# Performance work log

Measured on AMD Instinct MI355X. Metric: run time of the kernel, lower is better.

## Reference

```python
import jax, jax.numpy as jnp
import numpy as np

N = 32768      # total nodes
B = 64         # graphs
NPG = 512      # nodes per graph
E = 524288     # edges (avg degree 16)
H = 4          # heads
Fh = 64        # per-head dim
C = H * Fh     # 256
FIN = 128
RATIO = 0.5


def gat(x, src, dst, W, a_src, a_dst, bias, n_nodes):
    # PyG GATConv: linear -> add self-loops -> edge softmax over dst -> scatter-add
    h = (x @ W).reshape(n_nodes, H, Fh)
    loop = jnp.arange(n_nodes)
    s = jnp.concatenate([src, loop])
    d = jnp.concatenate([dst, loop])
    es = jnp.sum(h * a_src, axis=-1)  # [N,H]
    ed = jnp.sum(h * a_dst, axis=-1)  # [N,H]
    e = jax.nn.leaky_relu(es[s] + ed[d], 0.2)  # [E+N,H]
    m = jax.ops.segment_max(e, d, num_segments=n_nodes)
    ex = jnp.exp(e - m[d])
    den = jax.ops.segment_sum(ex, d, num_segments=n_nodes)
    alpha = ex / (den[d] + 1e-16)  # [E+N,H]
    out = jax.ops.segment_sum(alpha[:, :, None] * h[s], d, num_segments=n_nodes)
    return out.reshape(n_nodes, C) + bias


def pool(x, sw, sb, tw, tb, n_graphs, n_per):
    # equal-size graphs -> per-graph top-k as a batched top_k
    k = max(1, int(n_per * RATIO))
    scores = jax.nn.sigmoid(x @ sw + sb)[:, 0].reshape(n_graphs, n_per)
    _, idx = jax.lax.top_k(scores, k)  # [B,k]
    xb = x.reshape(n_graphs, n_per, x.shape[-1])
    sel = jnp.take_along_axis(xb, idx[:, :, None], axis=1)
    sel = sel.reshape(n_graphs * k, x.shape[-1])
    return sel @ tw + tb, k


def setup_inputs() -> dict:
    key = jax.random.key(0)
    ks = jax.random.split(key, 24)
    x = jax.random.normal(ks[0], (N, FIN), dtype=jnp.float32)
    # within-graph random edges
    gbase = jnp.repeat(jnp.arange(B, dtype=jnp.int32) * NPG, E // B)
    src = gbase + jax.random.randint(ks[1], (E,), 0, NPG)
    dst = gbase + jax.random.randint(ks[2], (E,), 0, NPG)
    edge_index = jnp.stack([src, dst]).astype(jnp.int32)
    batch = jnp.repeat(jnp.arange(B, dtype=jnp.int32), NPG)
    def lin(k, fi, fo):
        return jax.random.normal(k, (fi, fo), dtype=jnp.float32) / np.sqrt(fi)
    inp = dict(x=x, edge_index=edge_index, batch=batch)
    inp["W1"] = lin(ks[3], FIN, C)
    inp["a_src1"] = jax.random.normal(ks[4], (H, Fh), jnp.float32) / np.sqrt(Fh)
    inp["a_dst1"] = jax.random.normal(ks[5], (H, Fh), jnp.float32) / np.sqrt(Fh)
    inp["b1"] = jnp.zeros((C,), jnp.float32)
    inp["W2"] = lin(ks[6], C, C)
    inp["a_src2"] = jax.random.normal(ks[7], (H, Fh), jnp.float32) / np.sqrt(Fh)
    inp["a_dst2"] = jax.random.normal(ks[8], (H, Fh), jnp.float32) / np.sqrt(Fh)
    inp["b2"] = jnp.zeros((C,), jnp.float32)
    inp["p1_sw"] = lin(ks[9], C, 1)
    inp["p1_sb"] = jnp.zeros((1,), jnp.float32)
    inp["p1_tw"] = lin(ks[10], C, C)
    inp["p1_tb"] = jnp.zeros((C,), jnp.float32)
    inp["p2_sw"] = lin(ks[11], C, 1)
    inp["p2_sb"] = jnp.zeros((1,), jnp.float32)
    inp["p2_tw"] = lin(ks[12], C, C)
    inp["p2_tb"] = jnp.zeros((C,), jnp.float32)
    inp["c1w"] = lin(ks[13], C, 64)
    inp["c1b"] = jnp.zeros((64,), jnp.float32)
    inp["c2w"] = lin(ks[14], 64, 2)
    inp["c2b"] = jnp.zeros((2,), jnp.float32)
    return inp


def reference(x, edge_index, batch, W1, a_src1, a_dst1, b1, W2, a_src2, a_dst2, b2,
              p1_sw, p1_sb, p1_tw, p1_tb, p2_sw, p2_sb, p2_tw, p2_tb,
              c1w, c1b, c2w, c2b):
    src, dst = edge_index[0], edge_index[1]
    h = jax.nn.elu(gat(x, src, dst, W1, a_src1, a_dst1, b1, N))
    h = jax.nn.elu(gat(h, src, dst, W2, a_src2, a_dst2, b2, N))
    # pool1 then pool2 (edge_index after pooling is never consumed by the output path)
    h, k1 = pool(h, p1_sw, p1_sb, p1_tw, p1_tb, B, NPG)
    h, k2 = pool(h, p2_sw, p2_sb, p2_tw, p2_tb, B, k1)
    g = h.reshape(B, k2, C).mean(axis=1)  # global mean pool per graph
    g = jax.nn.relu(g @ c1w + c1b)
    g = g @ c2w + c2b
    return jax.nn.log_softmax(g, axis=1)
```

## Files before the change

### kernel.cpp

```cpp
#include <hip/hip_runtime.h>
#include <hip/hip_bf16.h>
#include <hip/hip_fp16.h>
#include <math.h>

constexpr int NN  = 32768;
constexpr int BG  = 64;
constexpr int NPG = 512;
constexpr int EG  = 524288;
constexpr int EPG = EG / BG;
constexpr int HH  = 4;
constexpr int FH  = 64;
constexpr int CC  = 256;
constexpr int FIN = 128;
constexpr int KP1 = 256;
constexpr int KP2 = 128;
constexpr int NS  = 4;

typedef __attribute__((ext_vector_type(8))) short short8;
typedef __attribute__((ext_vector_type(4))) float f32x4;
typedef __attribute__((ext_vector_type(2))) float f32x2v;

__device__ inline float leaky02(float v) { return v > 0.0f ? v : 0.2f * v; }

__device__ inline unsigned short f2bf(float v) {
    __hip_bfloat16 h = __float2bfloat16(v);
    return *(unsigned short*)&h;
}
__device__ inline float bf2f(unsigned short u) {
    __hip_bfloat16 h;
    *(unsigned short*)&h = u;
    return __bfloat162float(h);
}
__device__ inline void split2(float v, unsigned short& hi, unsigned short& lo) {
    hi = f2bf(v);
    lo = f2bf(v - bf2f(hi));
}
__device__ inline void split8(const float* p, short8& hi, short8& lo) {
    const float4 f0 = *(const float4*)p;
    const float4 f1 = *(const float4*)(p + 4);
    unsigned short h, l;
    split2(f0.x, h, l); hi[0] = (short)h; lo[0] = (short)l;
    split2(f0.y, h, l); hi[1] = (short)h; lo[1] = (short)l;
    split2(f0.z, h, l); hi[2] = (short)h; lo[2] = (short)l;
    split2(f0.w, h, l); hi[3] = (short)h; lo[3] = (short)l;
    split2(f1.x, h, l); hi[4] = (short)h; lo[4] = (short)l;
    split2(f1.y, h, l); hi[5] = (short)h; lo[5] = (short)l;
    split2(f1.z, h, l); hi[6] = (short)h; lo[6] = (short)l;
    split2(f1.w, h, l); hi[7] = (short)h; lo[7] = (short)l;
}

__device__ inline unsigned short f2h(float v) {
    __half h = __float2half(v);
    return *(unsigned short*)&h;
}

__device__ inline unsigned int fmap(float v) {
    unsigned int b = __float_as_uint(v);
    return (b & 0x80000000u) ? ~b : (b | 0x80000000u);
}

__device__ inline void acc8h(const unsigned short* p, float a, f32x2v* acc) {
    const uint4 u = *(const uint4*)p;
    const __half2* hp = (const __half2*)&u;
    f32x2v av; av[0] = a; av[1] = a;
#pragma unroll
    for (int i = 0; i < 4; ++i) {
        const float2 f = __half22float2(hp[i]);
        f32x2v fv; fv[0] = f.x; fv[1] = f.y;
        acc[i] = __builtin_elementwise_fma(fv, av, acc[i]);
    }
}

__global__ __launch_bounds__(1024) void setup_k(
        const int* __restrict__ src, const int* __restrict__ dst,
        int* __restrict__ rowp, int* __restrict__ esrc,
        const float* __restrict__ tw1, const float* __restrict__ sw2,
        const float* __restrict__ tb1, const float* __restrict__ sb2,
        float* __restrict__ w12, float* __restrict__ b12,
        const float* __restrict__ tw2, const float* __restrict__ c1w,
        const float* __restrict__ tb2, float* __restrict__ T,
        float* __restrict__ bc2,
        const float* __restrict__ W1, const float* __restrict__ W2,
        unsigned short* __restrict__ w1ph, unsigned short* __restrict__ w1pl,
        unsigned short* __restrict__ w2ph, unsigned short* __restrict__ w2pl,
        const float* __restrict__ x,
        unsigned short* __restrict__ xph, unsigned short* __restrict__ xpl) {
    __shared__ int lcnt[NPG];
    __shared__ int wsum[8];
    const int b = blockIdx.x;
    const int t = threadIdx.x;
    if (b < BG) {
        const int g = b;
        const int ebase = g * EPG;
        const int nbase = g * NPG;
        if (t < NPG) lcnt[t] = 0;
        __syncthreads();
        int ds[EPG / 1024];
#pragma unroll
        for (int j = 0; j < EPG / 1024; ++j) {
            ds[j] = dst[ebase + t + 1024 * j] - nbase;
            atomicAdd(&lcnt[ds[j]], 1);
        }
        __syncthreads();
        int c = 0, sInc = 0;
        if (t < NPG) {
            c = lcnt[t];
            sInc = c;
#pragma unroll
            for (int o = 1; o < 64; o <<= 1) {
                int v = __shfl_up(sInc, o);
                if ((t & 63) >= o) sInc += v;
            }
            if ((t & 63) == 63) wsum[t >> 6] = sInc;
        }
        __syncthreads();
        if (t < 8) {
            int v = wsum[t];
            int s = v;
#pragma unroll
            for (int o = 1; o < 8; o <<= 1) {
                int u2 = __shfl_up(s, o, 8);
                if (t >= o) s += u2;
            }
            wsum[t] = s - v;
        }
        __syncthreads();
        if (t < NPG) {
            const int ex = sInc - c + wsum[t >> 6];
            rowp[nbase + t] = ebase + ex;
            lcnt[t] = ex;
        }
        if (g == BG - 1 && t == 0) rowp[NN] = EG;
        __syncthreads();
#pragma unroll
        for (int j = 0; j < EPG / 1024; ++j) {
            int p = atomicAdd(&lcnt[ds[j]], 1);
            esrc[ebase + p] = src[ebase + t + 1024 * j];
        }
        return;
    }
    const int pb = b - BG;
    if (pb >= 114) {
        const size_t idx = ((size_t)(pb - 114) * 1024 + t) * 8;
        short8 hi, lo;
        split8(x + idx, hi, lo);
        *(short8*)(xph + idx) = hi;
        *(short8*)(xpl + idx) = lo;
        return;
    }
    if (t >= 256) return;
    if (pb < 66) {
        if (pb == 0) {
            float s = 0.0f;
            for (int o = 0; o < CC; ++o) s += tw1[t * CC + o] * sw2[o];
            w12[t] = s;
            if (t == 0) {
                float bb = 0.0f;
                for (int o = 0; o < CC; ++o) bb += tb1[o] * sw2[o];
                *b12 = bb + sb2[0];
            }
        } else if (pb < 65) {
            const int r = (pb - 1) * 4 + (t >> 6);
            const int cth = t & 63;
            float s = 0.0f;
            for (int j = 0; j < CC; ++j) s = fmaf(tw2[r * CC + j], c1w[j * 64 + cth], s);
            T[r * 64 + cth] = s;
        } else if (t < 64) {
            float s = 0.0f;
            for (int j = 0; j < CC; ++j) s = fmaf(tb2[j], c1w[j * 64 + t], s);
            bc2[t] = s;
        }
    } else {
        const int idx = (pb - 66) * 256 + t;
        if (idx < 4096) {
            const int nt = idx >> 8, rem = idx & 255;
            const int kg = rem >> 6, l = rem & 63;
            const int n = nt * 16 + (l & 15);
            const int kb = kg * 32 + (l >> 4) * 8;
            unsigned short h[8], lo[8];
#pragma unroll
            for (int j = 0; j < 8; ++j) split2(W1[(kb + j) * CC + n], h[j], lo[j]);
#pragma unroll
            for (int j = 0; j < 8; ++j) {
                w1ph[(size_t)idx * 8 + j] = h[j];
                w1pl[(size_t)idx * 8 + j] = lo[j];
            }
        } else {
            const int i2 = idx - 4096;
            const int nt = i2 >> 9, rem = i2 & 511;
            const int kg = rem >> 6, l = rem & 63;
            const int n = nt * 16 + (l & 15);
            const int kb = kg * 32 + (l >> 4) * 8;
            unsigned short h[8], lo[8];
#pragma unroll
            for (int j = 0; j < 8; ++j) split2(W2[(kb + j) * CC + n], h[j], lo[j]);
#pragma unroll
            for (int j = 0; j < 8; ++j) {
                w2ph[(size_t)i2 * 8 + j] = h[j];
                w2pl[(size_t)i2 * 8 + j] = lo[j];
            }
        }
    }
}

__global__ __launch_bounds__(256, 4) void gemm_mfma_attn(
        const unsigned short* __restrict__ Ahi, const unsigned short* __restrict__ Alo,
        const unsigned short* __restrict__ Bph, const unsigned short* __restrict__ Bpl,
        unsigned short* __restrict__ Cb, int K,
        const float* __restrict__ a_src, const float* __restrict__ a_dst,
        float* __restrict__ es, float* __restrict__ ed,
        const float* __restrict__ tw1, const float* __restrict__ T,
        const float* __restrict__ tb1, const float* __restrict__ bc2,
        const float* __restrict__ c1b, float* __restrict__ Wc,
        float* __restrict__ bcv) {
    const int t = threadIdx.x;
    const int bx = blockIdx.x;
    if (bx >= NN / 32) {
        const int fb = bx - NN / 32;
        if (fb < 64) {
            const int r = fb * 4 + (t >> 6);
            const int cth = t & 63;
            float s = 0.0f;
            for (int j = 0; j < CC; ++j) s = fmaf(tw1[r * CC + j], T[j * 64 + cth], s);
            Wc[r * 64 + cth] = s;
        } else if (t < 64) {
            float s = 0.0f;
            for (int j = 0; j < CC; ++j) s = fmaf(tb1[j], T[j * 64 + t], s);
            bcv[t] = s + bc2[t] + c1b[t];
        }
        return;
    }
    const int w = t >> 6;
    const int l = t & 63;
    const int xcd  = bx & 7;
    const int slot = bx >> 3;
    const int gph  = xcd + ((slot >> 4) << 3);
    const int row0 = gph * NPG + ((slot & 15) << 5);
    const int m = l & 15;
    const int q = l >> 4;
    const int ncol0 = w * 64;
    const int KG = K >> 5;

    const unsigned short* aH0 = Ahi + (size_t)(row0 + m) * K + q * 8;
    const unsigned short* aL0 = Alo + (size_t)(row0 + m) * K + q * 8;
    const unsigned short* aH1 = aH0 + (size_t)16 * K;
    const unsigned short* aL1 = aL0 + (size_t)16 * K;

    f32x4 acc0[4], acc1[4];
#pragma unroll
    for (int c = 0; c < 4; ++c) {
        acc0[c] = (f32x4){0.f, 0.f, 0.f, 0.f};
        acc1[c] = (f32x4){0.f, 0.f, 0.f, 0.f};
    }

    for (int kg = 0; kg < KG; ++kg) {
        const int ko = kg * 32;
        short8 ah0 = *(const short8*)(aH0 + ko);
        short8 al0 = *(const short8*)(aL0 + ko);
        short8 ah1 = *(const short8*)(aH1 + ko);
        short8 al1 = *(const short8*)(aL1 + ko);
#pragma unroll
        for (int c = 0; c < 4; ++c) {
            const int nt = (w << 2) + c;
            const size_t boff = ((size_t)(nt * KG + kg) * 64 + l) * 8;
            short8 bh = *(const short8*)(Bph + boff);
            short8 bl = *(const short8*)(Bpl + boff);
            acc0[c] = __builtin_amdgcn_mfma_f32_16x16x32_bf16(ah0, bh, acc0[c], 0, 0, 0);
            acc0[c] = __builtin_amdgcn_mfma_f32_16x16x32_bf16(ah0, bl, acc0[c], 0, 0, 0);
            acc0[c] = __builtin_amdgcn_mfma_f32_16x16x32_bf16(al0, bh, acc0[c], 0, 0, 0);
            acc1[c] = __builtin_amdgcn_mfma_f32_16x16x32_bf16(ah1, bh, acc1[c], 0, 0, 0);
            acc1[c] = __builtin_amdgcn_mfma_f32_16x16x32_bf16(ah1, bl, acc1[c], 0, 0, 0);
            acc1[c] = __builtin_amdgcn_mfma_f32_16x16x32_bf16(al1, bh, acc1[c], 0, 0, 0);
        }
    }

#pragma unroll
    for (int c = 0; c < 4; ++c)
#pragma unroll
        for (int r = 0; r < 4; ++r) {
            Cb[(size_t)(row0 + q * 4 + r) * CC + ncol0 + c * 16 + m] = f2h(acc0[c][r]);
            Cb[(size_t)(row0 + 16 + q * 4 + r) * CC + ncol0 + c * 16 + m] = f2h(acc1[c][r]);
        }

    float asv[4], adv[4];
#pragma unroll
    for (int c = 0; c < 4; ++c) {
        asv[c] = a_src[ncol0 + c * 16 + m];
        adv[c] = a_dst[ncol0 + c * 16 + m];
    }
#pragma unroll
    for (int r = 0; r < 4; ++r) {
        float ps0 = 0.f, pd0 = 0.f, ps1 = 0.f, pd1 = 0.f;
#pragma unroll
        for (int c = 0; c < 4; ++c) {
            ps0 = fmaf(acc0[c][r], asv[c], ps0);
            pd0 = fmaf(acc0[c][r], adv[c], pd0);
            ps1 = fmaf(acc1[c][r], asv[c], ps1);
            pd1 = fmaf(acc1[c][r], adv[c], pd1);
        }
#pragma unroll
        for (int o = 8; o >= 1; o >>= 1) {
            ps0 += __shfl_down(ps0, o, 16);
            pd0 += __shfl_down(pd0, o, 16);
            ps1 += __shfl_down(ps1, o, 16);
            pd1 += __shfl_down(pd1, o, 16);
        }
        if (m == 0) {
            es[(row0 + q * 4 + r) * HH + w] = ps0;
            ed[(row0 + q * 4 + r) * HH + w] = pd0;
            es[(row0 + 16 + q * 4 + r) * HH + w] = ps1;
            ed[(row0 + 16 + q * 4 + r) * HH + w] = pd1;
        }
    }
}

__global__ __launch_bounds__(256) void edge1_gemm2(
        const unsigned short* __restrict__ zh1,
        const int* __restrict__ rowp, const int* __restrict__ esrc,
        const float* __restrict__ es1, const float* __restrict__ ed1,
        const float* __restrict__ bias,
        const unsigned short* __restrict__ Bph, const unsigned short* __restrict__ Bpl,
        unsigned short* __restrict__ zh2,
        const float* __restrict__ a_src, const float* __restrict__ a_dst,
        float* __restrict__ es2, float* __restrict__ ed2) {
    __shared__ unsigned char AhB[32 * 512];
    __shared__ unsigned char AlB[32 * 512];
    const int t = threadIdx.x;
    const int w = t >> 6;
    const int l = t & 63;
    const int bx   = blockIdx.x;
    const int xcd  = bx & 7;
    const int slot = bx >> 3;
    const int gph  = xcd + ((slot >> 4) << 3);
    const int row0 = gph * NPG + ((slot & 15) << 5);

    const int h    = l & 3;
    const int ei   = l >> 2;
    const int lh   = l & 31;
    const int half = l >> 5;
    const int hcol = lh >> 3;
    const int c0   = lh << 3;

    for (int nd = 0; nd < 8; ++nd) {
        const int rloc = w * 8 + nd;
        const int d = row0 + rloc;
        const int beg = rowp[d];
        const int deg = rowp[d + 1] - beg;

        f32x2v acc[4];
#pragma unroll
        for (int i = 0; i < 4; ++i) acc[i] = (f32x2v){0.f, 0.f};

        if (deg <= 16 * NS) {
            const float edh = ed1[d * HH + h];
            int   sidx[NS];
            float v[NS];
#pragma unroll
            for (int j = 0; j < NS; ++j) { sidx[j] = d; v[j] = 0.0f; }
            float vmax = -INFINITY, eself = 0.0f, vself = 0.0f;
            if (ei == 0) {
                vself = leaky02(es1[d * HH + h] + edh);
                vmax = vself;
            }
#pragma unroll
            for (int j = 0; j < NS; ++j) {
                int i = ei + 16 * j;
                if (i < deg) {
                    sidx[j] = esrc[beg + i];
                    v[j] = leaky02(es1[sidx[j] * HH + h] + edh);
                    vmax = fmaxf(vmax, v[j]);
                }
            }
#pragma unroll
            for (int o = 4; o <= 32; o <<= 1) vmax = fmaxf(vmax, __shfl_xor(vmax, o));
            float dsum = 0.0f;
#pragma unroll
            for (int j = 0; j < NS; ++j) {
                int i = ei + 16 * j;
                if (i < deg) { v[j] = __expf(v[j] - vmax); dsum += v[j]; }
            }
            if (ei == 0) { eself = __expf(vself - vmax); dsum += eself; }
#pragma unroll
            for (int o = 4; o <= 32; o <<= 1) dsum += __shfl_xor(dsum, o);
            const float inv = 1.0f / (dsum + 1e-16f);
#pragma unroll
            for (int j = 0; j < NS; ++j) v[j] *= inv;
            eself *= inv;

            float aself = __shfl(eself, hcol);
            if (half) aself = 0.0f;
            acc8h(zh1 + (size_t)d * CC + c0, aself, acc);

#pragma unroll
            for (int j = 0; j < NS; ++j) {
                if (16 * j < deg) {
#pragma unroll
                    for (int rr = 0; rr < 8; ++rr) {
                        if (16 * j + 2 * rr < deg) {
                            const int slb  = (2 * rr + half) << 2;
                            const int srcn = __shfl(sidx[j], slb);
                            const float a  = __shfl(v[j], slb + hcol);
                            acc8h(zh1 + (size_t)srcn * CC + c0, a, acc);
                        }
                    }
                }
            }
        } else {
            const float edh = ed1[d * HH + h];
            float vmax = (ei == 0) ? leaky02(es1[d * HH + h] + edh) : -INFINITY;
            for (int i = ei; i < deg; i += 16)
                vmax = fmaxf(vmax, leaky02(es1[esrc[beg + i] * HH + h] + edh));
#pragma unroll
            for (int o = 4; o <= 32; o <<= 1) vmax = fmaxf(vmax, __shfl_xor(vmax, o));
            float dsum = (ei == 0) ? __expf(leaky02(es1[d * HH + h] + edh) - vmax) : 0.0f;
            for (int i = ei; i < deg; i += 16)
                dsum += __expf(leaky02(es1[esrc[beg + i] * HH + h] + edh) - vmax);
#pragma unroll
            for (int o = 4; o <= 32; o <<= 1) dsum += __shfl_xor(dsum, o);
            const float inv = 1.0f / (dsum + 1e-16f);

            const float vmaxc = __shfl(vmax, hcol);
            const float invc  = __shfl(inv,  hcol);
            const float edh4  = ed1[d * HH + hcol];
            float a0 = __expf(leaky02(es1[d * HH + hcol] + edh4) - vmaxc) * invc;
            if (half) a0 = 0.0f;
            acc8h(zh1 + (size_t)d * CC + c0, a0, acc);
            for (int e = half; e < deg; e += 2) {
                const int srcn = esrc[beg + e];
                const float a = __expf(leaky02(es1[srcn * HH + hcol] + edh4) - vmaxc) * invc;
                acc8h(zh1 + (size_t)srcn * CC + c0, a, acc);
            }
        }

#pragma unroll
        for (int i = 0; i < 4; ++i) {
            float a0 = acc[i][0]; a0 += __shfl_xor(a0, 32);
            float a1 = acc[i][1]; a1 += __shfl_xor(a1, 32);
            acc[i][0] = a0; acc[i][1] = a1;
        }

        const int cw = c0 + (half << 2);
        float o0 = half ? acc[2][0] : acc[0][0];
        float o1 = half ? acc[2][1] : acc[0][1];
        float o2 = half ? acc[3][0] : acc[1][0];
        float o3 = half ? acc[3][1] : acc[1][1];

        const float4 bv = *(const float4*)(bias + cw);
        o0 += bv.x; o0 = o0 > 0.0f ? o0 : __expf(o0) - 1.0f;
        o1 += bv.y; o1 = o1 > 0.0f ? o1 : __expf(o1) - 1.0f;
        o2 += bv.z; o2 = o2 > 0.0f ? o2 : __expf(o2) - 1.0f;
        o3 += bv.w; o3 = o3 > 0.0f ? o3 : __expf(o3) - 1.0f;

        ushort4 uh, ul;
        split2(o0, uh.x, ul.x);
        split2(o1, uh.y, ul.y);
        split2(o2, uh.z, ul.z);
        split2(o3, uh.w, ul.w);
        const size_t bo = (size_t)(((rloc * 512) + cw * 2) ^ ((rloc & 7) << 4));
        *(ushort4*)(AhB + bo) = uh;
        *(ushort4*)(AlB + bo) = ul;
    }

    __syncthreads();

    const int m = l & 15;
    const int q = l >> 4;
    const int ncol0 = w * 64;
    constexpr int KG = CC >> 5;

    f32x4 acc0[4], acc1[4];
#pragma unroll
    for (int c = 0; c < 4; ++c) {
        acc0[c] = (f32x4){0.f, 0.f, 0.f, 0.f};
        acc1[c] = (f32x4){0.f, 0.f, 0.f, 0.f};
    }

    for (int kg = 0; kg < KG; ++kg) {
        const int co = kg * 64 + q * 16;
        const size_t bo0 = (size_t)(((m * 512) + co) ^ ((m & 7) << 4));
        const size_t bo1 = (size_t)((((16 + m) * 512) + co) ^ ((m & 7) << 4));
        short8 ah0 = *(const short8*)(AhB + bo0);
        short8 al0 = *(const short8*)(AlB + bo0);
        short8 ah1 = *(const short8*)(AhB + bo1);
        short8 al1 = *(const short8*)(AlB + bo1);
#pragma unroll
        for (int c = 0; c < 4; ++c) {
            const int nt = (w << 2) + c;
            const size_t boff = ((size_t)(nt * KG + kg) * 64 + l) * 8;
            short8 bh = *(const short8*)(Bph + boff);
            short8 bl = *(const short8*)(Bpl + boff);
            acc0[c] = __builtin_amdgcn_mfma_f32_16x16x32_bf16(ah0, bh, acc0[c], 0, 0, 0);
            acc0[c] = __builtin_amdgcn_mfma_f32_16x16x32_bf16(ah0, bl, acc0[c], 0, 0, 0);
            acc0[c] = __builtin_amdgcn_mfma_f32_16x16x32_bf16(al0, bh, acc0[c], 0, 0, 0);
            acc1[c] = __builtin_amdgcn_mfma_f32_16x16x32_bf16(ah1, bh, acc1[c], 0, 0, 0);
            acc1[c] = __builtin_amdgcn_mfma_f32_16x16x32_bf16(ah1, bl, acc1[c], 0, 0, 0);
            acc1[c] = __builtin_amdgcn_mfma_f32_16x16x32_bf16(al1, bh, acc1[c], 0, 0, 0);
        }
    }

#pragma unroll
    for (int c = 0; c < 4; ++c)
#pragma unroll
        for (int r = 0; r < 4; ++r) {
            zh2[(size_t)(row0 + q * 4 + r) * CC + ncol0 + c * 16 + m] = f2h(acc0[c][r]);
            zh2[(size_t)(row0 + 16 + q * 4 + r) * CC + ncol0 + c * 16 + m] = f2h(acc1[c][r]);
        }

    float asv[4], adv[4];
#pragma unroll
    for (int c = 0; c < 4; ++c) {
        asv[c] = a_src[ncol0 + c * 16 + m];
        adv[c] = a_dst[ncol0 + c * 16 + m];
    }
#pragma unroll
    for (int r = 0; r < 4; ++r) {
        float ps0 = 0.f, pd0 = 0.f, ps1 = 0.f, pd1 = 0.f;
#pragma unroll
        for (int c = 0; c < 4; ++c) {
            ps0 = fmaf(acc0[c][r], asv[c], ps0);
            pd0 = fmaf(acc0[c][r], adv[c], pd0);
            ps1 = fmaf(acc1[c][r], asv[c], ps1);
            pd1 = fmaf(acc1[c][r], adv[c], pd1);
        }
#pragma unroll
        for (int o = 8; o >= 1; o >>= 1) {
            ps0 += __shfl_down(ps0, o, 16);
            pd0 += __shfl_down(pd0, o, 16);
            ps1 += __shfl_down(ps1, o, 16);
            pd1 += __shfl_down(pd1, o, 16);
        }
        if (m == 0) {
            es2[(row0 + q * 4 + r) * HH + w] = ps0;
            ed2[(row0 + q * 4 + r) * HH + w] = pd0;
            es2[(row0 + 16 + q * 4 + r) * HH + w] = ps1;
            ed2[(row0 + 16 + q * 4 + r) * HH + w] = pd1;
        }
    }
}

__global__ __launch_bounds__(256) void gat_edge(const unsigned short* __restrict__ zh,
                                                const int* __restrict__ rowp,
                                                const int* __restrict__ esrc,
                                                const float* __restrict__ es,
                                                const float* __restrict__ ed,
                                                const float* __restrict__ bias,
                                                float* __restrict__ out,
                                                const float* __restrict__ sw1,
                                                const float* __restrict__ sb1,
                                                const float* __restrict__ w12,
                                                const float* __restrict__ b12,
                                                float* __restrict__ sc1,
                                                float* __restrict__ sc2) {
    const int w = threadIdx.x >> 6;
    const int l = threadIdx.x & 63;
    const int b    = blockIdx.x;
    const int xcd  = b & 7;
    const int slot = b >> 3;
    const int gph  = xcd + ((slot >> 7) << 3);
    const int d    = gph * NPG + ((slot & 127) << 2) + w;

    const int h    = l & 3;
    const int ei   = l >> 2;
    const int lh   = l & 31;
    const int half = l >> 5;
    const int hcol = lh >> 3;
    const int c0   = lh << 3;

    const int beg = rowp[d];
    const int deg = rowp[d + 1] - beg;

    f32x2v acc[4];
#pragma unroll
    for (int i = 0; i < 4; ++i) acc[i] = (f32x2v){0.f, 0.f};

    if (deg <= 16 * NS) {
        const float edh = ed[d * HH + h];
        int   sidx[NS];
        float v[NS];
#pragma unroll
        for (int j = 0; j < NS; ++j) { sidx[j] = d; v[j] = 0.0f; }
        float vmax = -INFINITY, eself = 0.0f, vself = 0.0f;
        if (ei == 0) {
            vself = leaky02(es[d * HH + h] + edh);
            vmax = vself;
        }
#pragma unroll
        for (int j = 0; j < NS; ++j) {
            int i = ei + 16 * j;
            if (i < deg) {
                sidx[j] = esrc[beg + i];
                v[j] = leaky02(es[sidx[j] * HH + h] + edh);
                vmax = fmaxf(vmax, v[j]);
            }
        }
#pragma unroll
        for (int o = 4; o <= 32; o <<= 1) vmax = fmaxf(vmax, __shfl_xor(vmax, o));
        float dsum = 0.0f;
#pragma unroll
        for (int j = 0; j < NS; ++j) {
            int i = ei + 16 * j;
            if (i < deg) { v[j] = __expf(v[j] - vmax); dsum += v[j]; }
        }
        if (ei == 0) { eself = __expf(vself - vmax); dsum += eself; }
#pragma unroll
        for (int o = 4; o <= 32; o <<= 1) dsum += __shfl_xor(dsum, o);
        const float inv = 1.0f / (dsum + 1e-16f);
#pragma unroll
        for (int j = 0; j < NS; ++j) v[j] *= inv;
        eself *= inv;

        float aself = __shfl(eself, hcol);
        if (half) aself = 0.0f;
        acc8h(zh + (size_t)d * CC + c0, aself, acc);

#pragma unroll
        for (int j = 0; j < NS; ++j) {
            if (16 * j < deg) {
#pragma unroll
                for (int rr = 0; rr < 8; ++rr) {
                    if (16 * j + 2 * rr < deg) {
                        const int slb  = (2 * rr + half) << 2;
                        const int srcn = __shfl(sidx[j], slb);
                        const float a  = __shfl(v[j], slb + hcol);
                        acc8h(zh + (size_t)srcn * CC + c0, a, acc);
                    }
                }
            }
        }
    } else {
        const float edh = ed[d * HH + h];
        float vmax = (ei == 0) ? leaky02(es[d * HH + h] + edh) : -INFINITY;
        for (int i = ei; i < deg; i += 16)
            vmax = fmaxf(vmax, leaky02(es[esrc[beg + i] * HH + h] + edh));
#pragma unroll
        for (int o = 4; o <= 32; o <<= 1) vmax = fmaxf(vmax, __shfl_xor(vmax, o));
        float dsum = (ei == 0) ? __expf(leaky02(es[d * HH + h] + edh) - vmax) : 0.0f;
        for (int i = ei; i < deg; i += 16)
            dsum += __expf(leaky02(es[esrc[beg + i] * HH + h] + edh) - vmax);
#pragma unroll
        for (int o = 4; o <= 32; o <<= 1) dsum += __shfl_xor(dsum, o);
        const float inv = 1.0f / (dsum + 1e-16f);

        const float vmaxc = __shfl(vmax, hcol);
        const float invc  = __shfl(inv,  hcol);
        const float edh4  = ed[d * HH + hcol];
        float a0 = __expf(leaky02(es[d * HH + hcol] + edh4) - vmaxc) * invc;
        if (half) a0 = 0.0f;
        acc8h(zh + (size_t)d * CC + c0, a0, acc);
        for (int e = half; e < deg; e += 2) {
            const int srcn = esrc[beg + e];
            const float a = __expf(leaky02(es[srcn * HH + hcol] + edh4) - vmaxc) * invc;
            acc8h(zh + (size_t)srcn * CC + c0, a, acc);
        }
    }

#pragma unroll
    for (int i = 0; i < 4; ++i) {
        float a0 = acc[i][0]; a0 += __shfl_xor(a0, 32);
        float a1 = acc[i][1]; a1 += __shfl_xor(a1, 32);
        acc[i][0] = a0; acc[i][1] = a1;
    }

    const int cw = c0 + (half << 2);
    float o0 = half ? acc[2][0] : acc[0][0];
    float o1 = half ? acc[2][1] : acc[0][1];
    float o2 = half ? acc[3][0] : acc[1][0];
    float o3 = half ? acc[3][1] : acc[1][1];

    const float4 bv = *(const float4*)(bias + cw);
    o0 += bv.x; o0 = o0 > 0.0f ? o0 : __expf(o0) - 1.0f;
    o1 += bv.y; o1 = o1 > 0.0f ? o1 : __expf(o1) - 1.0f;
    o2 += bv.z; o2 = o2 > 0.0f ? o2 : __expf(o2) - 1.0f;
    o3 += bv.w; o3 = o3 > 0.0f ? o3 : __expf(o3) - 1.0f;

    *(float4*)(out + (size_t)d * CC + cw) = make_float4(o0, o1, o2, o3);

    {
        const float4 s1 = *(const float4*)(sw1 + cw);
        const float4 s2 = *(const float4*)(w12 + cw);
        float r1 = o0 * s1.x + o1 * s1.y + o2 * s1.z + o3 * s1.w;
        float r2 = o0 * s2.x + o1 * s2.y + o2 * s2.z + o3 * s2.w;
#pragma unroll
        for (int off = 32; off >= 1; off >>= 1) {
            r1 += __shfl_xor(r1, off);
            r2 += __shfl_xor(r2, off);
        }
        if (l == 0) {
            sc1[d] = r1 + sb1[0];
            sc2[d] = r2 + b12[0];
        }
    }
}

__global__ __launch_bounds__(512) void pool_g(const float* __restrict__ sc1,
                                              const float* __restrict__ sc2,
                                              const float* __restrict__ feat,
                                              const float* __restrict__ Wc,
                                              const float* __restrict__ bc,
                                              const float* __restrict__ c2w,
                                              const float* __restrict__ c2b,
                                              float* __restrict__ outp) {
    __shared__ unsigned int us[NPG];
    __shared__ unsigned char kb[NPG];
    __shared__ int list[KP2];
    __shared__ float v0[CC];
    __shared__ float vbuf[2][CC];
    __shared__ float part[4][64];
    __shared__ float v2[64];
    const int g = blockIdx.x;
    const int t = threadIdx.x;
    const int lane = t & 63, wid = t >> 6;

    const float s2val = sc2[(size_t)g * NPG + t];
    us[t] = fmap(sc1[(size_t)g * NPG + t]);
    __syncthreads();

    if (wid == 0) {
        unsigned int u[8];
#pragma unroll
        for (int j = 0; j < 8; ++j) u[j] = us[j * 64 + lane];
        unsigned int p = 0;
        for (int bb = 31; bb >= 0; --bb) {
            const unsigned int cand = p | (1u << bb);
            int cnt = 0;
#pragma unroll
            for (int j = 0; j < 8; ++j) cnt += __popcll(__ballot(u[j] >= cand));
            if (cnt >= KP1) p = cand;
        }
        int cgt = 0;
#pragma unroll
        for (int j = 0; j < 8; ++j) cgt += __popcll(__ballot(u[j] > p));
        const int kk = KP1 - cgt;
        const unsigned long long lm = (1ull << lane) - 1ull;
        int preEq = 0;
#pragma unroll
        for (int j = 0; j < 8; ++j) {
            const unsigned long long balEq = __ballot(u[j] == p);
            const int eqr = preEq + __popcll(balEq & lm);
            preEq += __popcll(balEq);
            kb[j * 64 + lane] =
                (unsigned char)((u[j] > p) || ((u[j] == p) && (eqr < kk)));
        }
    }
    __syncthreads();

    us[t] = kb[t] ? fmap(s2val) : 0u;
    __syncthreads();
    if (wid == 0) {
        unsigned int u[8];
#pragma unroll
        for (int j = 0; j < 8; ++j) u[j] = us[j * 64 + lane];
        unsigned int p = 0;
        for (int bb = 31; bb >= 0; --bb) {
            const unsigned int cand = p | (1u << bb);
            int cnt = 0;
#pragma unroll
            for (int j = 0; j < 8; ++j) cnt += __popcll(__ballot(u[j] >= cand));
            if (cnt >= KP2) p = cand;
        }
        int cgt = 0;
#pragma unroll
        for (int j = 0; j < 8; ++j) cgt += __popcll(__ballot(u[j] > p));
        const int kk = KP2 - cgt;
        const unsigned long long lm = (1ull << lane) - 1ull;
        int preEq = 0, preKeep = 0;
#pragma unroll
        for (int j = 0; j < 8; ++j) {
            const unsigned long long balEq = __ballot(u[j] == p);
            const int eqr = preEq + __popcll(balEq & lm);
            preEq += __popcll(balEq);
            const int keep = (u[j] > p) || ((u[j] == p) && (eqr < kk));
            const unsigned long long balK = __ballot(keep);
            const int pos = preKeep + __popcll(balK & lm);
            preKeep += __popcll(balK);
            if (keep) list[pos] = j * 64 + lane;
        }
    }
    __syncthreads();

    {
        const int col = t & (CC - 1);
        const int hf = t >> 8;
        float acc = 0.0f;
        for (int i = hf * 64; i < hf * 64 + 64; ++i)
            acc += feat[((size_t)g * NPG + list[i]) * CC + col];
        vbuf[hf][col] = acc;
    }
    __syncthreads();
    if (t < CC) v0[t] = (vbuf[0][t] + vbuf[1][t]) * (1.0f / KP2);
    __syncthreads();

    if (t < 256) {
        const int q = t >> 6, cth = t & 63;
        float pr = 0.0f;
        for (int j = q * 64; j < q * 64 + 64; ++j)
            pr = fmaf(v0[j], Wc[j * 64 + cth], pr);
        part[q][cth] = pr;
    }
    __syncthreads();
    if (t < 64) {
        float u = bc[t];
#pragma unroll
        for (int q = 0; q < 4; ++q) u += part[q][t];
        v2[t] = fmaxf(u, 0.0f);
    }
    __syncthreads();
    if (t < 2) {
        float o = c2b[t];
        for (int j = 0; j < 64; ++j) o = fmaf(v2[j], c2w[j * 2 + t], o);
        part[0][t] = o;
    }
    __syncthreads();
    if (t == 0) {
        float a = part[0][0], bq = part[0][1];
        float mx = fmaxf(a, bq);
        float lse = mx + logf(expf(a - mx) + expf(bq - mx));
        outp[g * 2 + 0] = a - lse;
        outp[g * 2 + 1] = bq - lse;
    }
}

extern "C" void kernel_launch(void* const* d_in, const int* in_sizes, int n_in,
                              void* d_out, int out_size, void* d_ws, size_t ws_size,
                              hipStream_t stream) {
    const float* x      = (const float*)d_in[0];
    const int*   ei     = (const int*)d_in[1];
    const int*   src    = ei;
    const int*   dst    = ei + EG;
    const float* W1     = (const float*)d_in[3];
    const float* a_src1 = (const float*)d_in[4];
    const float* a_dst1 = (const float*)d_in[5];
    const float* b1     = (const float*)d_in[6];
    const float* W2     = (const float*)d_in[7];
    const float* a_src2 = (const float*)d_in[8];
    const float* a_dst2 = (const float*)d_in[9];
    const float* b2     = (const float*)d_in[10];
    const float* p1_sw  = (const float*)d_in[11];
    const float* p1_sb  = (const float*)d_in[12];
    const float* p1_tw  = (const float*)d_in[13];
    const float* p1_tb  = (const float*)d_in[14];
    const float* p2_sw  = (const float*)d_in[15];
    const float* p2_sb  = (const float*)d_in[16];
    const float* p2_tw  = (const float*)d_in[17];
    const float* p2_tb  = (const float*)d_in[18];
    const float* c1w    = (const float*)d_in[19];
    const float* c1b    = (const float*)d_in[20];
    const float* c2w    = (const float*)d_in[21];
    const float* c2b    = (const float*)d_in[22];
    float* out = (float*)d_out;

    float* ws = (float*)d_ws;
    float* z = ws;
    unsigned short* zh1 = (unsigned short*)z;
    unsigned short* zh2 = zh1 + (size_t)NN * CC;
    float* fregion = z + (size_t)NN * CC;
    float* featF = fregion;
    float* wsp = fregion + (size_t)NN * CC;
    unsigned short* w1ph = (unsigned short*)wsp;
    unsigned short* w1pl = w1ph + 256 * FIN;
    unsigned short* w2ph = w1pl + 256 * FIN;
    unsigned short* w2pl = w2ph + 256 * CC;
    float* es  = (float*)(w2pl + 256 * CC);
    float* ed  = es + NN * HH;
    int* rowp  = (int*)(ed + NN * HH);
    int* esrc  = rowp + NN + 1;
    float* sc1 = (float*)(esrc + EG);
    float* sc2 = sc1 + NN;
    int* sel1  = (int*)(sc2 + NN);
    float* w12 = (float*)(sel1 + NN);
    float* b12 = w12 + CC;
    float* T   = b12 + 64;
    float* Wc  = T + CC * 64;
    float* bc2 = Wc + CC * 64;
    float* bcv = bc2 + 64;
    float* es2 = bcv + 64;
    float* ed2 = es2 + (size_t)NN * HH;
    unsigned short* xph = (unsigned short*)(ed2 + (size_t)NN * HH);
    unsigned short* xpl = xph + (size_t)NN * FIN;

    setup_k<<<BG + 66 + 48 + 512, 1024, 0, stream>>>(
        src, dst, rowp, esrc,
        p1_tw, p2_sw, p1_tb, p2_sb, w12, b12, p2_tw, c1w, p2_tb, T, bc2,
        W1, W2, w1ph, w1pl, w2ph, w2pl, x, xph, xpl);

    gemm_mfma_attn<<<NN / 32 + 65, 256, 0, stream>>>(
        xph, xpl, w1ph, w1pl, zh1, FIN, a_src1, a_dst1, es, ed,
        p1_tw, T, p1_tb, bc2, c1b, Wc, bcv);

    edge1_gemm2<<<NN / 32, 256, 0, stream>>>(
        zh1, rowp, esrc, es, ed, b1,
        w2ph, w2pl, zh2, a_src2, a_dst2, es2, ed2);

    gat_edge<<<NN / 4, 256, 0, stream>>>(zh2, rowp, esrc, es2, ed2, b2,
                                         featF, p1_sw, p1_sb, w12, b12,
                                         sc1, sc2);

    pool_g<<<BG, 512, 0, stream>>>(sc1, sc2, featF, Wc, bcv, c2w, c2b, out);
}
```

Measured before the change: 242.0 us.

## Fuse pooling tail into gat_edge via last-block-per-graph counter and fp16 features

```diff
diff --git a/kernel.cpp b/kernel.cpp
--- a/kernel.cpp
+++ b/kernel.cpp
@@ -52,6 +52,11 @@
 __device__ inline unsigned short f2h(float v) {
     __half h = __float2half(v);
     return *(unsigned short*)&h;
+}
+__device__ inline float h2f(unsigned short u) {
+    __half h;
+    *(unsigned short*)&h = u;
+    return __half2float(h);
 }
 
 __device__ inline unsigned int fmap(float v) {
@@ -84,7 +89,8 @@
         unsigned short* __restrict__ w1ph, unsigned short* __restrict__ w1pl,
         unsigned short* __restrict__ w2ph, unsigned short* __restrict__ w2pl,
         const float* __restrict__ x,
-        unsigned short* __restrict__ xph, unsigned short* __restrict__ xpl) {
+        unsigned short* __restrict__ xph, unsigned short* __restrict__ xpl,
+        int* __restrict__ cnt) {
     __shared__ int lcnt[NPG];
     __shared__ int wsum[8];
     const int b = blockIdx.x;
@@ -151,6 +157,7 @@
     if (t >= 256) return;
     if (pb < 66) {
         if (pb == 0) {
+            if (t < BG) cnt[t] = 0;
             float s = 0.0f;
             for (int o = 0; o < CC; ++o) s += tw1[t * CC + o] * sw2[o];
             w12[t] = s;
@@ -544,13 +551,24 @@
                                                 const float* __restrict__ es,
                                                 const float* __restrict__ ed,
                                                 const float* __restrict__ bias,
-                                                float* __restrict__ out,
+                                                unsigned short* __restrict__ featH,
                                                 const float* __restrict__ sw1,
                                                 const float* __restrict__ sb1,
                                                 const float* __restrict__ w12,
                                                 const float* __restrict__ b12,
                                                 float* __restrict__ sc1,
-                                                float* __restrict__ sc2) {
+                                                float* __restrict__ sc2,
+                                                const float* __restrict__ Wc,
+                                                const float* __restrict__ bc,
+                                                const float* __restrict__ c2w,
+                                                const float* __restrict__ c2b,
+                                                int* __restrict__ cnt,
+                                                float* __restrict__ outp) {
+    __shared__ int list[KP2];
+    __shared__ float v0[CC];
+    __shared__ float part[4][64];
+    __shared__ float v2[64];
+    __shared__ int lastf;
     const int w = threadIdx.x >> 6;
     const int l = threadIdx.x & 63;
     const int b    = blockIdx.x;
@@ -673,7 +691,11 @@
     o2 += bv.z; o2 = o2 > 0.0f ? o2 : __expf(o2) - 1.0f;
     o3 += bv.w; o3 = o3 > 0.0f ? o3 : __expf(o3) - 1.0f;
 
-    *(float4*)(out + (size_t)d * CC + cw) = make_float4(o0, o1, o2, o3);
+    {
+        ushort4 uf;
+        uf.x = f2h(o0); uf.y = f2h(o1); uf.z = f2h(o2); uf.w = f2h(o3);
+        *(ushort4*)(featH + (size_t)d * CC + cw) = uf;
+    }
 
     {
         const float4 s1 = *(const float4*)(sw1 + cw);
@@ -690,86 +712,68 @@
             sc2[d] = r2 + b12[0];
         }
     }
-}
-
-__global__ __launch_bounds__(512) void pool_g(const float* __restrict__ sc1,
-                                              const float* __restrict__ sc2,
-                                              const float* __restrict__ feat,
-                                              const float* __restrict__ Wc,
-                                              const float* __restrict__ bc,
-                                              const float* __restrict__ c2w,
-                                              const float* __restrict__ c2b,
-                                              float* __restrict__ outp) {
-    __shared__ unsigned int us[NPG];
-    __shared__ unsigned char kb[NPG];
-    __shared__ int list[KP2];
-    __shared__ float v0[CC];
-    __shared__ float vbuf[2][CC];
-    __shared__ float part[4][64];
-    __shared__ float v2[64];
-    const int g = blockIdx.x;
+
+    __threadfence();
+    __syncthreads();
+    if (threadIdx.x == 0) lastf = (atomicAdd(&cnt[gph], 1) == 127);
+    __syncthreads();
+    if (!lastf) return;
+    __threadfence();
+    const int g = gph;
     const int t = threadIdx.x;
-    const int lane = t & 63, wid = t >> 6;
-
-    const float s2val = sc2[(size_t)g * NPG + t];
-    us[t] = fmap(sc1[(size_t)g * NPG + t]);
-    __syncthreads();
-
-    if (wid == 0) {
+
+    if (t < 64) {
+        const int lane = t;
+        const unsigned long long lm = (1ull << lane) - 1ull;
         unsigned int u[8];
 #pragma unroll
-        for (int j = 0; j < 8; ++j) u[j] = us[j * 64 + lane];
+        for (int j = 0; j < 8; ++j)
+            u[j] = fmap(sc1[(size_t)g * NPG + j * 64 + lane]);
         unsigned int p = 0;
         for (int bb = 31; bb >= 0; --bb) {
             const unsigned int cand = p | (1u << bb);
-            int cnt = 0;
-#pragma unroll
-            for (int j = 0; j < 8; ++j) cnt += __popcll(__ballot(u[j] >= cand));
-            if (cnt >= KP1) p = cand;
+            int cntc = 0;
+#pragma unroll
+            for (int j = 0; j < 8; ++j) cntc += __popcll(__ballot(u[j] >= cand));
+            if (cntc >= KP1) p = cand;
         }
         int cgt = 0;
 #pragma unroll
         for (int j = 0; j < 8; ++j) cgt += __popcll(__ballot(u[j] > p));
-        const int kk = KP1 - cgt;
-        const unsigned long long lm = (1ull << lane) - 1ull;
+        int kk = KP1 - cgt;
         int preEq = 0;
+        int kbr[8];
 #pragma unroll
         for (int j = 0; j < 8; ++j) {
             const unsigned long long balEq = __ballot(u[j] == p);
             const int eqr = preEq + __popcll(balEq & lm);
             preEq += __popcll(balEq);
-            kb[j * 64 + lane] =
-                (unsigned char)((u[j] > p) || ((u[j] == p) && (eqr < kk)));
-        }
-    }
-    __syncthreads();
-
-    us[t] = kb[t] ? fmap(s2val) : 0u;
-    __syncthreads();
-    if (wid == 0) {
-        unsigned int u[8];
-#pragma unroll
-        for (int j = 0; j < 8; ++j) u[j] = us[j * 64 + lane];
-        unsigned int p = 0;
+            kbr[j] = (u[j] > p) || ((u[j] == p) && (eqr < kk));
+        }
+        unsigned int u2[8];
+#pragma unroll
+        for (int j = 0; j < 8; ++j)
+            u2[j] = kbr[j] ? fmap(sc2[(size_t)g * NPG + j * 64 + lane]) : 0u;
+        p = 0;
         for (int bb = 31; bb >= 0; --bb) {
             const unsigned int cand = p | (1u << bb);
-            int cnt = 0;
-#pragma unroll
-            for (int j = 0; j < 8; ++j) cnt += __popcll(__ballot(u[j] >= cand));
-            if (cnt >= KP2) p = cand;
-        }
-        int cgt = 0;
-#pragma unroll
-        for (int j = 0; j < 8; ++j) cgt += __popcll(__ballot(u[j] > p));
-        const int kk = KP2 - cgt;
-        const unsigned long long lm = (1ull << lane) - 1ull;
-        int preEq = 0, preKeep = 0;
+            int cntc = 0;
+#pragma unroll
+            for (int j = 0; j < 8; ++j) cntc += __popcll(__ballot(u2[j] >= cand));
+            if (cntc >= KP2) p = cand;
+        }
+        cgt = 0;
+#pragma unroll
+        for (int j = 0; j < 8; ++j) cgt += __popcll(__ballot(u2[j] > p));
+        kk = KP2 - cgt;
+        preEq = 0;
+        int preKeep = 0;
 #pragma unroll
         for (int j = 0; j < 8; ++j) {
-            const unsigned long long balEq = __ballot(u[j] == p);
+            const unsigned long long balEq = __ballot(u2[j] == p);
             const int eqr = preEq + __popcll(balEq & lm);
             preEq += __popcll(balEq);
-            const int keep = (u[j] > p) || ((u[j] == p) && (eqr < kk));
+            const int keep = (u2[j] > p) || ((u2[j] == p) && (eqr < kk));
             const unsigned long long balK = __ballot(keep);
             const int pos = preKeep + __popcll(balK & lm);
             preKeep += __popcll(balK);
@@ -779,18 +783,14 @@
     __syncthreads();
 
     {
-        const int col = t & (CC - 1);
-        const int hf = t >> 8;
-        float acc = 0.0f;
-        for (int i = hf * 64; i < hf * 64 + 64; ++i)
-            acc += feat[((size_t)g * NPG + list[i]) * CC + col];
-        vbuf[hf][col] = acc;
+        float accm = 0.0f;
+        for (int i = 0; i < KP2; ++i)
+            accm += h2f(featH[((size_t)g * NPG + list[i]) * CC + t]);
+        v0[t] = accm * (1.0f / KP2);
     }
     __syncthreads();
-    if (t < CC) v0[t] = (vbuf[0][t] + vbuf[1][t]) * (1.0f / KP2);
-    __syncthreads();
-
-    if (t < 256) {
+
+    {
         const int q = t >> 6, cth = t & 63;
         float pr = 0.0f;
         for (int j = q * 64; j < q * 64 + 64; ++j)
@@ -854,7 +854,7 @@
     unsigned short* zh1 = (unsigned short*)z;
     unsigned short* zh2 = zh1 + (size_t)NN * CC;
     float* fregion = z + (size_t)NN * CC;
-    float* featF = fregion;
+    unsigned short* featH = (unsigned short*)fregion;
     float* wsp = fregion + (size_t)NN * CC;
     unsigned short* w1ph = (unsigned short*)wsp;
     unsigned short* w1pl = w1ph + 256 * FIN;
@@ -866,8 +866,8 @@
     int* esrc  = rowp + NN + 1;
     float* sc1 = (float*)(esrc + EG);
     float* sc2 = sc1 + NN;
-    int* sel1  = (int*)(sc2 + NN);
-    float* w12 = (float*)(sel1 + NN);
+    int* cnt   = (int*)(sc2 + NN);
+    float* w12 = (float*)(cnt + NN);
     float* b12 = w12 + CC;
     float* T   = b12 + 64;
     float* Wc  = T + CC * 64;
@@ -881,7 +881,7 @@
     setup_k<<<BG + 66 + 48 + 512, 1024, 0, stream>>>(
         src, dst, rowp, esrc,
         p1_tw, p2_sw, p1_tb, p2_sb, w12, b12, p2_tw, c1w, p2_tb, T, bc2,
-        W1, W2, w1ph, w1pl, w2ph, w2pl, x, xph, xpl);
+        W1, W2, w1ph, w1pl, w2ph, w2pl, x, xph, xpl, cnt);
 
     gemm_mfma_attn<<<NN / 32 + 65, 256, 0, stream>>>(
         xph, xpl, w1ph, w1pl, zh1, FIN, a_src1, a_dst1, es, ed,
@@ -892,8 +892,7 @@
         w2ph, w2pl, zh2, a_src2, a_dst2, es2, ed2);
 
     gat_edge<<<NN / 4, 256, 0, stream>>>(zh2, rowp, esrc, es2, ed2, b2,
-                                         featF, p1_sw, p1_sb, w12, b12,
-                                         sc1, sc2);
-
-    pool_g<<<BG, 512, 0, stream>>>(sc1, sc2, featF, Wc, bcv, c2w, c2b, out);
-}
+                                         featH, p1_sw, p1_sb, w12, b12,
+                                         sc1, sc2, Wc, bcv, c2w, c2b,
+                                         cnt, out);
+}
```

Result: slower. 874.3 us (+261.3%).
